# Optimization experiments

Hardware: AMD Instinct MI355X
Metric: run time of the kernel (lower is better)

## Reference

```python
import jax, jax.numpy as jnp
import numpy as np

H = 768  # hidden size
L = 2    # num layers


def _lstm_layer(xs, ms, Wih, Whh, bih, bhh):
    """xs: [S,B,in], ms: [S,B,H] mask. Returns (outputs [S,B,H], (hT, cT)).
    PyTorch LSTMCell gate order: i, f, g, o. Zero initial state (module default),
    so the reset term init_hidden*(1-mask) is identically zero."""
    B = xs.shape[1]
    h0 = jnp.zeros((B, H), xs.dtype)
    c0 = jnp.zeros((B, H), xs.dtype)
    # Precompute input projections for all timesteps in one big GEMM.
    x_proj = jnp.einsum('sbi,gi->sbg', xs, Wih) + bih + bhh  # [S,B,4H]

    def step(carry, inp):
        h, c = carry
        xp, mt = inp
        gates = xp + h @ Whh.T  # [B,4H]
        i, f, g, o = jnp.split(gates, 4, axis=-1)
        i = jax.nn.sigmoid(i)
        f = jax.nn.sigmoid(f)
        g = jnp.tanh(g)
        o = jax.nn.sigmoid(o)
        c_next = (f * c + i * g)
        h_next = o * jnp.tanh(c_next)
        # mask-based state reset (h0=c0=0 -> pure multiply)
        h_next = h_next * mt
        c_next = c_next * mt
        return (h_next, c_next), h_next

    (hT, cT), outs = jax.lax.scan(step, (h0, c0), (x_proj, ms))
    return outs, (hT, cT)


def setup_inputs() -> dict:
    key = jax.random.key(0)
    ks = jax.random.split(key, 5)
    s = 0.05
    return {
        'x': jax.random.normal(ks[0], (64, 512, 768), jnp.float32),
        'mask': jnp.ones((64, 512), jnp.float32),
        'W_ih': jax.random.normal(ks[1], (L, 4 * H, 768), jnp.float32) * s,
        'W_hh': jax.random.normal(ks[2], (L, 4 * H, H), jnp.float32) * s,
        'b_ih': jax.random.normal(ks[3], (L, 4 * H), jnp.float32) * s,
        'b_hh': jax.random.normal(ks[4], (L, 4 * H), jnp.float32) * s,
    }


def reference(x, mask, W_ih, W_hh, b_ih, b_hh):
    # batch_first=True: transpose to [S,B,...]
    xs = jnp.transpose(x, (1, 0, 2))          # [S,B,in]
    ms = jnp.transpose(mask, (1, 0))[:, :, None]  # [S,B,1]
    ms = jnp.broadcast_to(ms, ms.shape[:2] + (H,))  # [S,B,H]
    hn, cn = [], []
    inp = xs
    for l in range(L):
        outs, (hT, cT) = _lstm_layer(inp, ms, W_ih[l], W_hh[l], b_ih[l], b_hh[l])
        hn.append(hT)
        cn.append(cT)
        inp = outs
    output = jnp.transpose(inp, (1, 0, 2))  # [B,S,H]
    return output, (jnp.stack(hn, 0), jnp.stack(cn, 0))
```

## Files before the change

kernel.cpp:

```cpp
#include <hip/hip_runtime.h>
#include <hip/hip_bf16.h>


#define HID 768
#define FH  3072
#define SEQ 512
#define BAT 64
#define GB  16
#define WPG 64
#define CPW 12
#define NWG 256
#define TPB 768

typedef __attribute__((ext_vector_type(8))) __bf16 bf16x8;
typedef __attribute__((ext_vector_type(4))) float f32x4;
typedef unsigned int u32;

__device__ __forceinline__ float sigm(float z) { return 1.f / (1.f + __expf(-z)); }
__device__ __forceinline__ float tanh_fast(float x) {
  float a = fabsf(x);
  float e = __expf(-2.f * a);
  float t = (1.f - e) / (1.f + e);
  return copysignf(t, x);
}
__device__ __forceinline__ unsigned short bfbits(__bf16 b) {
  union { __bf16 b; unsigned short s; } u; u.b = b; return u.s;
}
__device__ __forceinline__ __bf16 bits2bf(unsigned short s) {
  union { unsigned short s; __bf16 b; } u; u.s = s; return u.b;
}
__device__ __forceinline__ u32 packsplit(float v) {
  __bf16 h = (__bf16)v;
  __bf16 l = (__bf16)(v - (float)h);
  return ((u32)bfbits(h) << 16) | (u32)bfbits(l);
}
__device__ __forceinline__ void split8(const float* p, bf16x8& hi, bf16x8& lo) {
  const float4* q = (const float4*)p;
  float4 a = q[0], b = q[1];
  float v[8] = {a.x, a.y, a.z, a.w, b.x, b.y, b.z, b.w};
#pragma unroll
  for (int i = 0; i < 8; ++i) {
    __bf16 h = (__bf16)v[i];
    hi[i] = h;
    lo[i] = (__bf16)(v[i] - (float)h);
  }
}
__device__ __forceinline__ void unpack8(const u32 w[8], bf16x8& hi, bf16x8& lo) {
#pragma unroll
  for (int i = 0; i < 8; ++i) {
    hi[i] = bits2bf((unsigned short)(w[i] >> 16));
    lo[i] = bits2bf((unsigned short)(w[i] & 0xffffu));
  }
}

template<int FMT>
__device__ __forceinline__ f32x4 proj384(const float* xf, const u32* xp,
                                         size_t base,
                                         const bf16x8* ah, const bf16x8* al) {
  f32x4 acc[4];
#pragma unroll
  for (int r = 0; r < 4; ++r) acc[r] = f32x4{0.f, 0.f, 0.f, 0.f};
#pragma unroll
  for (int kk = 0; kk < 12; ++kk) {
    bf16x8 bhi, blo;
    if constexpr (FMT == 0) {
      split8(xf + base + kk*32, bhi, blo);
    } else {
      const uint4* p = (const uint4*)(xp + base + kk*32);
      uint4 A = p[0], B = p[1];
      u32 w[8] = {A.x, A.y, A.z, A.w, B.x, B.y, B.z, B.w};
      unpack8(w, bhi, blo);
    }
    acc[(3*kk+0)&3] = __builtin_amdgcn_mfma_f32_16x16x32_bf16(ah[kk], bhi, acc[(3*kk+0)&3], 0, 0, 0);
    acc[(3*kk+1)&3] = __builtin_amdgcn_mfma_f32_16x16x32_bf16(al[kk], bhi, acc[(3*kk+1)&3], 0, 0, 0);
    acc[(3*kk+2)&3] = __builtin_amdgcn_mfma_f32_16x16x32_bf16(ah[kk], blo, acc[(3*kk+2)&3], 0, 0, 0);
  }
  return acc[0] + acc[1] + acc[2] + acc[3];
}

template<int XFMT, int WRITE_OUT>
__attribute__((amdgpu_waves_per_eu(3, 3)))
__global__ void __launch_bounds__(TPB)
lstm_scan(const float* __restrict__ xf,
          const u32* __restrict__ xp,
          const float* __restrict__ mask,
          const float* __restrict__ Wih,
          const float* __restrict__ Whh,
          const float* __restrict__ bih,
          const float* __restrict__ bhh,
          u32* __restrict__ hstream,
          float* __restrict__ out_f,
          float* __restrict__ hn,
          float* __restrict__ cn,
          int* __restrict__ flags)
{
  __shared__ f32x4 xacc_l[24][3][64];
  __shared__ f32x4 xpart_l[3][64];
  __shared__ f32x4 hpart_l[2][3][64];

  const int wg  = blockIdx.x;
  const int grp = wg >> 6;
  const int wid = wg & 63;
  const int tid = threadIdx.x;
  const int wv  = tid >> 6;
  const int l   = tid & 63;
  const int l15 = l & 15;
  const int lhi = l >> 4;

  const bool isx  = (wv < 6);
  const int lane6 = isx ? wv : (wv - 6);
  const int tile  = lane6 >> 1;
  const int half  = lane6 & 1;
  const int kofs  = half * 384;

  const int colA = wid*CPW + tile*4 + (l15 >> 2);
  const int qA   = l15 & 3;
  const float* wrow = (isx ? Wih : Whh) + (size_t)(qA*HID + colA)*HID + kofs + lhi*8;
  bf16x8 ah[12], al[12];
#pragma unroll
  for (int kk = 0; kk < 12; ++kk) split8(wrow + kk*32, ah[kk], al[kk]);

  const int batch = grp*GB + l15;
  const int colO  = wid*CPW + tile*4 + lhi;
  float bias4[4] = {0.f, 0.f, 0.f, 0.f};
  if (!isx && half == 1) {
#pragma unroll
    for (int j = 0; j < 4; ++j) bias4[j] = bih[j*HID + colO] + bhh[j*HID + colO];
  }
  const float* mrow = mask + batch*SEQ;
  int* gflags = flags + grp*WPG;

  const int kb = kofs + lhi*8;

  float cstate = 0.f;

  {
    f32x4 px{0.f, 0.f, 0.f, 0.f};
    if (isx) {
      size_t base = (XFMT == 0) ? ((size_t)batch*SEQ)*HID + kb
                                : ((size_t)batch)*HID + kb;
      px = proj384<XFMT>(xf, xp, base, ah, al);
      if (half == 0) xpart_l[tile][l] = px;
    }
    __syncthreads();
    if (isx && half == 1) xacc_l[0][tile][l] = px + xpart_l[tile][l];
    __syncthreads();
  }

#pragma unroll 1
  for (int s = 0; s < SEQ; ++s) {
    f32x4 xa{0.f, 0.f, 0.f, 0.f};
    if (isx && s + 1 < SEQ) {
      size_t base = (XFMT == 0) ? ((size_t)batch*SEQ + (s+1))*HID + kb
                                : ((size_t)(s+1)*BAT + batch)*HID + kb;
      xa = proj384<XFMT>(xf, xp, base, ah, al);
      if (half == 0) xpart_l[tile][l] = xa;
    }
    if (!isx && lane6 == 0 && s > 0) {
      while (true) {
        int v = __hip_atomic_load(gflags + l, __ATOMIC_RELAXED, __HIP_MEMORY_SCOPE_AGENT);
        if (__all(v >= s)) break;
        __builtin_amdgcn_s_sleep(1);
      }
    }
    __syncthreads();

    f32x4 ha{0.f, 0.f, 0.f, 0.f};
    if (!isx && s > 0) {
      size_t base = ((size_t)(s-1)*BAT + batch)*HID + kb;
      ha = proj384<1>(nullptr, hstream, base, ah, al);
      if (half == 0) hpart_l[s & 1][tile][l] = ha;
    }
    if (isx && half == 1 && s + 1 < SEQ)
      xacc_l[(s+1) & 3][tile][l] = xa + xpart_l[tile][l];
    __syncthreads();

    if (!isx && half == 1) {
      f32x4 z = xacc_l[s & 3][tile][l];
      if (s > 0) z = z + ha + hpart_l[s & 1][tile][l];
      float zi = z[0] + bias4[0], zf = z[1] + bias4[1];
      float zg = z[2] + bias4[2], zo = z[3] + bias4[3];
      float iv = sigm(zi), fv = sigm(zf), gv = tanh_fast(zg), ov = sigm(zo);
      float c  = fv*cstate + iv*gv;
      float hv = ov * tanh_fast(c);
      float m  = mrow[s];
      hv *= m; c *= m; cstate = c;

      u32 hw = packsplit(hv);
      __hip_atomic_store(hstream + ((size_t)s*BAT + batch)*HID + colO, hw,
                         __ATOMIC_RELAXED, __HIP_MEMORY_SCOPE_AGENT);
      if constexpr (WRITE_OUT) {
        __builtin_nontemporal_store(hv, out_f + ((size_t)batch*SEQ + s)*HID + colO);
      }
      if (s == SEQ - 1) {
        hn[batch*HID + colO] = hv;
        cn[batch*HID + colO] = c;
      }
      asm volatile("s_waitcnt vmcnt(0)" ::: "memory");
    }
    __syncthreads();
    if (tid == 0)
      __hip_atomic_store(gflags + wid, s + 1,
                         __ATOMIC_RELAXED, __HIP_MEMORY_SCOPE_AGENT);
  }
}

extern "C" void kernel_launch(void* const* d_in, const int* in_sizes, int n_in,
                              void* d_out, int out_size, void* d_ws, size_t ws_size,
                              hipStream_t stream) {
  const float* x    = (const float*)d_in[0];
  const float* mask = (const float*)d_in[1];
  const float* Wih  = (const float*)d_in[2];
  const float* Whh  = (const float*)d_in[3];
  const float* bih  = (const float*)d_in[4];
  const float* bhh  = (const float*)d_in[5];
  float* out = (float*)d_out;

  char* ws = (char*)d_ws;
  const size_t STREAM_B = (size_t)SEQ * BAT * HID * sizeof(u32);
  u32* opk   = (u32*)(ws);
  u32* hpk   = (u32*)(ws + STREAM_B);
  int* flags = (int*)(ws + 2*STREAM_B);

  (void)hipMemsetAsync(flags, 0, 2*NWG*sizeof(int), stream);

  float* hn = out + 25165824;
  float* cn = out + 25165824 + 98304;

  lstm_scan<0, 0><<<dim3(NWG), dim3(TPB), 0, stream>>>(
      x, nullptr, mask, Wih, Whh, bih, bhh,
      opk, nullptr, hn, cn, flags);

  lstm_scan<1, 1><<<dim3(NWG), dim3(TPB), 0, stream>>>(
      nullptr, opk, mask,
      Wih + (size_t)FH*HID, Whh + (size_t)FH*HID, bih + FH, bhh + FH,
      hpk, out, hn + 49152, cn + 49152, flags + NWG);
}
```

Before: 11.58 ms.

## Stream pre-packed recurrent weights from memory instead of holding them in registers

Adds a pre-pass kernel that splits W_hh into bf16 hi/lo pairs and packs them in MFMA-lane order in workspace. The recurrent waves now load these packed fragments from memory on every timestep instead of keeping them resident in registers, which lowers register pressure on those waves. In exchange, each step issues extra global/L2 loads on the serial critical path. When the workspace is too small, the second layer's hidden-state stream falls back to a two-slot ring read with atomic loads.

```diff
diff --git a/kernel.cpp b/kernel.cpp
--- a/kernel.cpp
+++ b/kernel.cpp
@@ -11,10 +11,12 @@
 #define CPW 12
 #define NWG 256
 #define TPB 768
+#define WBLK (12*64*8)
 
 typedef __attribute__((ext_vector_type(8))) __bf16 bf16x8;
 typedef __attribute__((ext_vector_type(4))) float f32x4;
 typedef unsigned int u32;
+typedef unsigned long long u64;
 
 __device__ __forceinline__ float sigm(float z) { return 1.f / (1.f + __expf(-z)); }
 __device__ __forceinline__ float tanh_fast(float x) {
@@ -51,6 +53,35 @@
     hi[i] = bits2bf((unsigned short)(w[i] >> 16));
     lo[i] = bits2bf((unsigned short)(w[i] & 0xffffu));
   }
+}
+__device__ __forceinline__ bf16x8 q2b(uint4 q) {
+  union { uint4 q; bf16x8 v; } u; u.q = q; return u.v;
+}
+__device__ __forceinline__ uint4 b2q(bf16x8 v) {
+  union { bf16x8 v; uint4 q; } u; u.v = v; return u.q;
+}
+
+__global__ void pack_wh(const float* __restrict__ Whh, u32* __restrict__ wpk) {
+  const int NT = 2*64*6*12*64;
+  int t = blockIdx.x * blockDim.x + threadIdx.x;
+  if (t >= NT) return;
+  int lane = t & 63; int r = t >> 6;
+  int kk = r % 12;  r /= 12;
+  int lane6 = r % 6; r /= 6;
+  int wid = r % 64; r /= 64;
+  int layer = r;
+  int tile = lane6 >> 1, half = lane6 & 1;
+  int l15 = lane & 15, lhi = lane >> 4;
+  int colA = wid*CPW + tile*4 + (l15 >> 2);
+  int qA   = l15 & 3;
+  int row  = qA*HID + colA;
+  int k    = half*384 + kk*32 + lhi*8;
+  const float* W = Whh + (size_t)layer*FH*HID;
+  bf16x8 hi, lo;
+  split8(W + (size_t)row*HID + k, hi, lo);
+  u32* dst = wpk + (size_t)t * 8;
+  *(uint4*)dst       = b2q(hi);
+  *(uint4*)(dst + 4) = b2q(lo);
 }
 
 template<int FMT>
@@ -78,17 +109,18 @@
   return acc[0] + acc[1] + acc[2] + acc[3];
 }
 
-template<int XFMT, int WRITE_OUT>
+template<int XFMT, int WRITE_OUT, int RING>
 __attribute__((amdgpu_waves_per_eu(3, 3)))
 __global__ void __launch_bounds__(TPB)
 lstm_scan(const float* __restrict__ xf,
           const u32* __restrict__ xp,
           const float* __restrict__ mask,
           const float* __restrict__ Wih,
-          const float* __restrict__ Whh,
+          const u32* __restrict__ whpk,
           const float* __restrict__ bih,
           const float* __restrict__ bhh,
-          u32* __restrict__ hstream,
+          u32* __restrict__ hdst,
+          const u32* __restrict__ hsrc,
           float* __restrict__ out_f,
           float* __restrict__ hn,
           float* __restrict__ cn,
@@ -115,10 +147,13 @@
 
   const int colA = wid*CPW + tile*4 + (l15 >> 2);
   const int qA   = l15 & 3;
-  const float* wrow = (isx ? Wih : Whh) + (size_t)(qA*HID + colA)*HID + kofs + lhi*8;
   bf16x8 ah[12], al[12];
-#pragma unroll
-  for (int kk = 0; kk < 12; ++kk) split8(wrow + kk*32, ah[kk], al[kk]);
+  if (isx) {
+    const float* wrow = Wih + (size_t)(qA*HID + colA)*HID + kofs + lhi*8;
+#pragma unroll
+    for (int kk = 0; kk < 12; ++kk) split8(wrow + kk*32, ah[kk], al[kk]);
+  }
+  const u32* wbh = whpk + ((size_t)wid*6 + lane6) * WBLK;
 
   const int batch = grp*GB + l15;
   const int colO  = wid*CPW + tile*4 + lhi;
@@ -167,8 +202,38 @@
 
     f32x4 ha{0.f, 0.f, 0.f, 0.f};
     if (!isx && s > 0) {
-      size_t base = ((size_t)(s-1)*BAT + batch)*HID + kb;
-      ha = proj384<1>(nullptr, hstream, base, ah, al);
+      size_t base = RING ? ((size_t)((s-1) & 1)*BAT + batch)*HID + kb
+                         : ((size_t)(s-1)*BAT + batch)*HID + kb;
+      f32x4 acc[4];
+#pragma unroll
+      for (int r = 0; r < 4; ++r) acc[r] = f32x4{0.f, 0.f, 0.f, 0.f};
+#pragma unroll
+      for (int kk = 0; kk < 12; ++kk) {
+        const uint4* wp = (const uint4*)(wbh + (size_t)(kk*64 + l)*8);
+        bf16x8 Ah = q2b(wp[0]);
+        bf16x8 Al = q2b(wp[1]);
+        u32 w[8];
+        if constexpr (RING) {
+          const u64* sp = (const u64*)(hsrc + base + kk*32);
+          u64 a = __hip_atomic_load(sp,     __ATOMIC_RELAXED, __HIP_MEMORY_SCOPE_AGENT);
+          u64 b = __hip_atomic_load(sp + 1, __ATOMIC_RELAXED, __HIP_MEMORY_SCOPE_AGENT);
+          u64 c = __hip_atomic_load(sp + 2, __ATOMIC_RELAXED, __HIP_MEMORY_SCOPE_AGENT);
+          u64 d = __hip_atomic_load(sp + 3, __ATOMIC_RELAXED, __HIP_MEMORY_SCOPE_AGENT);
+          w[0]=(u32)a; w[1]=(u32)(a>>32); w[2]=(u32)b; w[3]=(u32)(b>>32);
+          w[4]=(u32)c; w[5]=(u32)(c>>32); w[6]=(u32)d; w[7]=(u32)(d>>32);
+        } else {
+          const uint4* p = (const uint4*)(hsrc + base + kk*32);
+          uint4 A = p[0], B = p[1];
+          w[0]=A.x; w[1]=A.y; w[2]=A.z; w[3]=A.w;
+          w[4]=B.x; w[5]=B.y; w[6]=B.z; w[7]=B.w;
+        }
+        bf16x8 bhi, blo;
+        unpack8(w, bhi, blo);
+        acc[(3*kk+0)&3] = __builtin_amdgcn_mfma_f32_16x16x32_bf16(Ah, bhi, acc[(3*kk+0)&3], 0, 0, 0);
+        acc[(3*kk+1)&3] = __builtin_amdgcn_mfma_f32_16x16x32_bf16(Al, bhi, acc[(3*kk+1)&3], 0, 0, 0);
+        acc[(3*kk+2)&3] = __builtin_amdgcn_mfma_f32_16x16x32_bf16(Ah, blo, acc[(3*kk+2)&3], 0, 0, 0);
+      }
+      ha = acc[0] + acc[1] + acc[2] + acc[3];
       if (half == 0) hpart_l[s & 1][tile][l] = ha;
     }
     if (isx && half == 1 && s + 1 < SEQ)
@@ -187,7 +252,9 @@
       hv *= m; c *= m; cstate = c;
 
       u32 hw = packsplit(hv);
-      __hip_atomic_store(hstream + ((size_t)s*BAT + batch)*HID + colO, hw,
+      size_t wrow = RING ? ((size_t)(s & 1)*BAT + batch)*HID + colO
+                         : ((size_t)s*BAT + batch)*HID + colO;
+      __hip_atomic_store(hdst + wrow, hw,
                          __ATOMIC_RELAXED, __HIP_MEMORY_SCOPE_AGENT);
       if constexpr (WRITE_OUT) {
         __builtin_nontemporal_store(hv, out_f + ((size_t)batch*SEQ + s)*HID + colO);
@@ -217,22 +284,36 @@
   float* out = (float*)d_out;
 
   char* ws = (char*)d_ws;
-  const size_t STREAM_B = (size_t)SEQ * BAT * HID * sizeof(u32);
-  u32* opk   = (u32*)(ws);
-  u32* hpk   = (u32*)(ws + STREAM_B);
-  int* flags = (int*)(ws + 2*STREAM_B);
+  const size_t WPKH_B  = (size_t)2*64*6*WBLK*4;
+  const size_t STREAM_B = (size_t)SEQ*BAT*HID*4;
+  const size_t RING_B  = (size_t)2*BAT*HID*4;
+
+  u32* wpk = (u32*)ws;
+  u32* opk = (u32*)(ws + WPKH_B);
+  const bool big = ws_size >= WPKH_B + 2*STREAM_B + RING_B + 65536;
+  u32* h1  = (u32*)(ws + WPKH_B + STREAM_B);
+  int* flags = big ? (int*)(ws + WPKH_B + 2*STREAM_B)
+                   : (int*)(ws + WPKH_B + STREAM_B + RING_B);
 
   (void)hipMemsetAsync(flags, 0, 2*NWG*sizeof(int), stream);
+  pack_wh<<<2304, 256, 0, stream>>>(Whh, wpk);
 
   float* hn = out + 25165824;
   float* cn = out + 25165824 + 98304;
 
-  lstm_scan<0, 0><<<dim3(NWG), dim3(TPB), 0, stream>>>(
-      x, nullptr, mask, Wih, Whh, bih, bhh,
-      opk, nullptr, hn, cn, flags);
-
-  lstm_scan<1, 1><<<dim3(NWG), dim3(TPB), 0, stream>>>(
-      nullptr, opk, mask,
-      Wih + (size_t)FH*HID, Whh + (size_t)FH*HID, bih + FH, bhh + FH,
-      hpk, out, hn + 49152, cn + 49152, flags + NWG);
-}
+  const size_t WLH = (size_t)64*6*WBLK;
+
+  lstm_scan<0, 0, 0><<<dim3(NWG), dim3(TPB), 0, stream>>>(
+      x, nullptr, mask, Wih, wpk, bih, bhh,
+      opk, opk, nullptr, hn, cn, flags);
+
+  if (big) {
+    lstm_scan<1, 1, 0><<<dim3(NWG), dim3(TPB), 0, stream>>>(
+        nullptr, opk, mask, Wih + (size_t)FH*HID, wpk + WLH, bih + FH, bhh + FH,
+        h1, h1, out, hn + 49152, cn + 49152, flags + NWG);
+  } else {
+    lstm_scan<1, 1, 1><<<dim3(NWG), dim3(TPB), 0, stream>>>(
+        nullptr, opk, mask, Wih + (size_t)FH*HID, wpk + WLH, bih + FH, bhh + FH,
+        h1, h1, out, hn + 49152, cn + 49152, flags + NWG);
+  }
+}
```

New measurement: 13.67 ms. 1.18x slower.

## Fuse both LSTM layers into one persistent launch pipelined across timesteps

Applied to the files above, without the earlier changes.

Replaces the two sequential per-layer kernel launches with one launch of twice as many workgroups. The second half computes layer 1 and spin-waits on layer 0's per-step flags, so layer 1 runs one step behind layer 0 instead of after it finishes. The goal is to overlap the two serial recurrences and roughly halve the critical path. In exchange, every thread now holds both the Wih and Whh split weight fragments in registers while occupancy is raised to 6 waves per EU, which risks register spills. The scheme also depends on all 512 workgroups being co-resident, otherwise the spin-waits can deadlock.

```diff
diff --git a/kernel.cpp b/kernel.cpp
--- a/kernel.cpp
+++ b/kernel.cpp
@@ -78,29 +78,30 @@
   return acc[0] + acc[1] + acc[2] + acc[3];
 }
 
-template<int XFMT, int WRITE_OUT>
-__attribute__((amdgpu_waves_per_eu(3, 3)))
+__attribute__((amdgpu_waves_per_eu(6, 6)))
 __global__ void __launch_bounds__(TPB)
-lstm_scan(const float* __restrict__ xf,
-          const u32* __restrict__ xp,
-          const float* __restrict__ mask,
-          const float* __restrict__ Wih,
-          const float* __restrict__ Whh,
-          const float* __restrict__ bih,
-          const float* __restrict__ bhh,
-          u32* __restrict__ hstream,
-          float* __restrict__ out_f,
-          float* __restrict__ hn,
-          float* __restrict__ cn,
-          int* __restrict__ flags)
+lstm_fused(const float* __restrict__ x,
+           const float* __restrict__ mask,
+           const float* __restrict__ Wih,
+           const float* __restrict__ Whh,
+           const float* __restrict__ bih,
+           const float* __restrict__ bhh,
+           u32* __restrict__ opk,
+           u32* __restrict__ hpk,
+           float* __restrict__ out_f,
+           float* __restrict__ hn,
+           float* __restrict__ cn,
+           int* __restrict__ flags)
 {
-  __shared__ f32x4 xacc_l[24][3][64];
+  __shared__ f32x4 xacc_l[4][3][64];
   __shared__ f32x4 xpart_l[3][64];
   __shared__ f32x4 hpart_l[2][3][64];
 
   const int wg  = blockIdx.x;
-  const int grp = wg >> 6;
-  const int wid = wg & 63;
+  const bool LY1 = (wg >= NWG);
+  const int lwg = wg & (NWG - 1);
+  const int grp = lwg >> 6;
+  const int wid = lwg & 63;
   const int tid = threadIdx.x;
   const int wv  = tid >> 6;
   const int l   = tid & 63;
@@ -113,23 +114,33 @@
   const int half  = lane6 & 1;
   const int kofs  = half * 384;
 
+  const size_t loff = LY1 ? (size_t)FH*HID : 0;
+  const float* Wih_l = Wih + loff;
+  const float* Whh_l = Whh + loff;
+  const float* bih_l = bih + (LY1 ? FH : 0);
+  const float* bhh_l = bhh + (LY1 ? FH : 0);
+  u32* hstream = LY1 ? hpk : opk;
+  int* gflags  = flags + (LY1 ? NWG : 0) + grp*WPG;
+  int* gflags0 = flags + grp*WPG;
+
   const int colA = wid*CPW + tile*4 + (l15 >> 2);
   const int qA   = l15 & 3;
-  const float* wrow = (isx ? Wih : Whh) + (size_t)(qA*HID + colA)*HID + kofs + lhi*8;
-  bf16x8 ah[12], al[12];
-#pragma unroll
-  for (int kk = 0; kk < 12; ++kk) split8(wrow + kk*32, ah[kk], al[kk]);
+  const float* wih_row = Wih_l + (size_t)(qA*HID + colA)*HID + kofs + lhi*8;
+  const float* whh_row = Whh_l + (size_t)(qA*HID + colA)*HID + kofs + lhi*8;
+  bf16x8 ah[12], al[12], ahh[12], alh[12];
+#pragma unroll
+  for (int kk = 0; kk < 12; ++kk) split8(wih_row + kk*32, ah[kk],  al[kk]);
+#pragma unroll
+  for (int kk = 0; kk < 12; ++kk) split8(whh_row + kk*32, ahh[kk], alh[kk]);
 
   const int batch = grp*GB + l15;
   const int colO  = wid*CPW + tile*4 + lhi;
   float bias4[4] = {0.f, 0.f, 0.f, 0.f};
   if (!isx && half == 1) {
 #pragma unroll
-    for (int j = 0; j < 4; ++j) bias4[j] = bih[j*HID + colO] + bhh[j*HID + colO];
+    for (int r = 0; r < 4; ++r) bias4[r] = bih_l[r*HID + colO] + bhh_l[r*HID + colO];
   }
   const float* mrow = mask + batch*SEQ;
-  int* gflags = flags + grp*WPG;
-
   const int kb = kofs + lhi*8;
 
   float cstate = 0.f;
@@ -137,9 +148,16 @@
   {
     f32x4 px{0.f, 0.f, 0.f, 0.f};
     if (isx) {
-      size_t base = (XFMT == 0) ? ((size_t)batch*SEQ)*HID + kb
-                                : ((size_t)batch)*HID + kb;
-      px = proj384<XFMT>(xf, xp, base, ah, al);
+      if (LY1) {
+        while (true) {
+          int v = __hip_atomic_load(gflags0 + l, __ATOMIC_RELAXED, __HIP_MEMORY_SCOPE_AGENT);
+          if (__all(v >= 1)) break;
+          __builtin_amdgcn_s_sleep(4);
+        }
+        px = proj384<1>(nullptr, opk, ((size_t)batch)*HID + kb, ah, al);
+      } else {
+        px = proj384<0>(x, nullptr, ((size_t)batch*SEQ)*HID + kb, ah, al);
+      }
       if (half == 0) xpart_l[tile][l] = px;
     }
     __syncthreads();
@@ -151,9 +169,16 @@
   for (int s = 0; s < SEQ; ++s) {
     f32x4 xa{0.f, 0.f, 0.f, 0.f};
     if (isx && s + 1 < SEQ) {
-      size_t base = (XFMT == 0) ? ((size_t)batch*SEQ + (s+1))*HID + kb
-                                : ((size_t)(s+1)*BAT + batch)*HID + kb;
-      xa = proj384<XFMT>(xf, xp, base, ah, al);
+      if (LY1) {
+        while (true) {
+          int v = __hip_atomic_load(gflags0 + l, __ATOMIC_RELAXED, __HIP_MEMORY_SCOPE_AGENT);
+          if (__all(v >= s + 2)) break;
+          __builtin_amdgcn_s_sleep(2);
+        }
+        xa = proj384<1>(nullptr, opk, ((size_t)(s+1)*BAT + batch)*HID + kb, ah, al);
+      } else {
+        xa = proj384<0>(x, nullptr, ((size_t)batch*SEQ + (s+1))*HID + kb, ah, al);
+      }
       if (half == 0) xpart_l[tile][l] = xa;
     }
     if (!isx && lane6 == 0 && s > 0) {
@@ -167,8 +192,7 @@
 
     f32x4 ha{0.f, 0.f, 0.f, 0.f};
     if (!isx && s > 0) {
-      size_t base = ((size_t)(s-1)*BAT + batch)*HID + kb;
-      ha = proj384<1>(nullptr, hstream, base, ah, al);
+      ha = proj384<1>(nullptr, hstream, ((size_t)(s-1)*BAT + batch)*HID + kb, ahh, alh);
       if (half == 0) hpart_l[s & 1][tile][l] = ha;
     }
     if (isx && half == 1 && s + 1 < SEQ)
@@ -189,12 +213,14 @@
       u32 hw = packsplit(hv);
       __hip_atomic_store(hstream + ((size_t)s*BAT + batch)*HID + colO, hw,
                          __ATOMIC_RELAXED, __HIP_MEMORY_SCOPE_AGENT);
-      if constexpr (WRITE_OUT) {
+      if (LY1) {
         __builtin_nontemporal_store(hv, out_f + ((size_t)batch*SEQ + s)*HID + colO);
       }
       if (s == SEQ - 1) {
-        hn[batch*HID + colO] = hv;
-        cn[batch*HID + colO] = c;
+        float* hnl = hn + (LY1 ? 49152 : 0);
+        float* cnl = cn + (LY1 ? 49152 : 0);
+        hnl[batch*HID + colO] = hv;
+        cnl[batch*HID + colO] = c;
       }
       asm volatile("s_waitcnt vmcnt(0)" ::: "memory");
     }
@@ -227,12 +253,6 @@
   float* hn = out + 25165824;
   float* cn = out + 25165824 + 98304;
 
-  lstm_scan<0, 0><<<dim3(NWG), dim3(TPB), 0, stream>>>(
-      x, nullptr, mask, Wih, Whh, bih, bhh,
-      opk, nullptr, hn, cn, flags);
-
-  lstm_scan<1, 1><<<dim3(NWG), dim3(TPB), 0, stream>>>(
-      nullptr, opk, mask,
-      Wih + (size_t)FH*HID, Whh + (size_t)FH*HID, bih + FH, bhh + FH,
-      hpk, out, hn + 49152, cn + 49152, flags + NWG);
-}
+  lstm_fused<<<dim3(2*NWG), dim3(TPB), 0, stream>>>(
+      x, mask, Wih, Whh, bih, bhh, opk, hpk, out, hn, cn, flags);
+}
```

Measured after the change: 19.09 ms. 64.9% more time.
